# Kernel tuning notes

Measured on AMD Instinct MI355X. Metric: run time of the kernel, lower is better.

Reference implementation:

```python
import jax, jax.numpy as jnp
import numpy as np

KV_CACHE_SIZE = 8192
DIM = 128
BBPM_MEM_SIZE = 131072
B, T = 32, 8192
N_TOKENS = B * T  # 262144


def setup_inputs() -> dict:
    key = jax.random.key(0)
    k1, k2, k3 = jax.random.split(key, 3)
    keys = jax.random.randint(k1, (B, T), 0, 1000000, dtype=jnp.int64)
    values = jax.random.normal(k2, (B, T, DIM), dtype=jnp.float32)
    positions = jnp.arange(N_TOKENS, dtype=jnp.int64).reshape(B, T)
    query_keys = jax.random.randint(k3, (B, T), 0, 1000000, dtype=jnp.int64)
    query_positions = jax.random.randint(
        jax.random.fold_in(key, 7), (B, T), 0, N_TOKENS, dtype=jnp.int64)
    bbpm_mem = jnp.zeros((BBPM_MEM_SIZE, DIM), dtype=jnp.float32)
    return {"keys": keys, "values": values, "positions": positions,
            "query_keys": query_keys, "query_positions": query_positions,
            "bbpm_mem": bbpm_mem}


def reference(keys, values, positions, query_keys, query_positions, bbpm_mem):
    # --- write_to_cache ---
    keys_f = keys.reshape(-1)                  # [n]
    vals_f = values.reshape(-1, DIM)           # [n, d]
    pos_f = positions.reshape(-1)              # [n]
    n = keys_f.shape[0]

    # BBPM write: hashed additive associative memory (scatter-add).
    mem = bbpm_mem.at[keys_f % BBPM_MEM_SIZE].add(vals_f)

    # Ring-cache write: cache_ptr starts at 0 and K | n, so the sequential
    # overwrite loop leaves exactly the last K tokens: slot idx holds token
    # i = n - K + idx. (Original writes values into both k_cache and v_cache;
    # only v_cache is read.)
    K = KV_CACHE_SIZE
    v_cache = vals_f[n - K:]                   # [K, d]
    cache_positions = pos_f[n - K:]            # [K], unique

    # --- retrieve ---
    qkeys = query_keys.reshape(-1)             # [Q]
    qpos = query_positions.reshape(-1)         # [Q]

    # Position -> cache-slot map (positions are unique, so scatter-set is
    # equivalent to taking the first matching slot).
    pos_table = jnp.full((N_TOKENS,), -1, dtype=jnp.int32)
    pos_table = pos_table.at[cache_positions].set(
        jnp.arange(K, dtype=jnp.int32))
    idx = pos_table[qpos]                      # [Q]
    hit = idx >= 0

    cache_vals = v_cache[jnp.maximum(idx, 0)]          # [Q, d]
    bbpm_vals = mem[qkeys % BBPM_MEM_SIZE]             # [Q, d]
    out = jnp.where(hit[:, None], cache_vals, bbpm_vals)  # [Q, d]
    return out
```

## Files before the change

### kernel.cpp

```cpp
#include <hip/hip_runtime.h>


constexpr int DIM    = 128;
constexpr int MEM    = 131072;
constexpr int KCACHE = 8192;
constexpr int CAP    = 16;

__device__ __forceinline__ float4 ldrow(const float* __restrict__ p, int q) {
    return *reinterpret_cast<const float4*>(p + q * 4);
}

__global__ void fill_kernel(const int* __restrict__ keys,
                            int* __restrict__ cnt,
                            int* __restrict__ bucket,
                            int* __restrict__ ovf_cnt,
                            int* __restrict__ ovf,
                            int n) {
    int i = blockIdx.x * 256 + threadIdx.x;
    if (i >= n) return;
    int slot = ((unsigned)keys[i]) & (MEM - 1);
    int pos = atomicAdd(&cnt[slot], 1);
    if (pos < CAP) {
        bucket[slot * CAP + pos] = i;
    } else {
        int k = atomicAdd(ovf_cnt, 1);
        ovf[k] = i;
    }
}

__global__ void build_pos_kernel(const int* __restrict__ positions,
                                 int* __restrict__ pos_table, int n, int K) {
    int j = blockIdx.x * 256 + threadIdx.x;
    if (j >= K) return;
    int p = positions[n - K + j];
    if (p >= 0 && p < n) pos_table[p] = j;
}

__global__ void reduce_kernel(const float* __restrict__ vals,
                              const float* __restrict__ bbpm,
                              const int* __restrict__ cnt,
                              const int* __restrict__ bucket,
                              float* __restrict__ acc) {
    int g = threadIdx.x >> 5;
    int q = threadIdx.x & 31;
    int s0 = blockIdx.x * 16 + g;
    int s1 = s0 + 8;

    int c0 = cnt[s0]; if (c0 > CAP) c0 = CAP;
    int c1 = cnt[s1]; if (c1 > CAP) c1 = CAP;
    int4 b0 = reinterpret_cast<const int4*>(bucket)[s0 * 4];
    int4 b1 = reinterpret_cast<const int4*>(bucket)[s1 * 4];

    int r00 = c0 > 0 ? b0.x : 0, r01 = c0 > 1 ? b0.y : 0;
    int r10 = c1 > 0 ? b1.x : 0, r11 = c1 > 1 ? b1.y : 0;
    float m00 = c0 > 0 ? 1.f : 0.f, m01 = c0 > 1 ? 1.f : 0.f;
    float m10 = c1 > 0 ? 1.f : 0.f, m11 = c1 > 1 ? 1.f : 0.f;

    float4 A0  = ldrow(bbpm + (size_t)s0  * DIM, q);
    float4 A1  = ldrow(bbpm + (size_t)s1  * DIM, q);
    float4 V00 = ldrow(vals + (size_t)r00 * DIM, q);
    float4 V01 = ldrow(vals + (size_t)r01 * DIM, q);
    float4 V10 = ldrow(vals + (size_t)r10 * DIM, q);
    float4 V11 = ldrow(vals + (size_t)r11 * DIM, q);

    float4 a0, a1;
    a0.x = A0.x + m00 * V00.x + m01 * V01.x;
    a0.y = A0.y + m00 * V00.y + m01 * V01.y;
    a0.z = A0.z + m00 * V00.z + m01 * V01.z;
    a0.w = A0.w + m00 * V00.w + m01 * V01.w;
    a1.x = A1.x + m10 * V10.x + m11 * V11.x;
    a1.y = A1.y + m10 * V10.y + m11 * V11.y;
    a1.z = A1.z + m10 * V10.z + m11 * V11.z;
    a1.w = A1.w + m10 * V10.w + m11 * V11.w;

    if (c0 > 2) {
        float4 v = ldrow(vals + (size_t)b0.z * DIM, q);
        a0.x += v.x; a0.y += v.y; a0.z += v.z; a0.w += v.w;
        if (c0 > 3) {
            v = ldrow(vals + (size_t)b0.w * DIM, q);
            a0.x += v.x; a0.y += v.y; a0.z += v.z; a0.w += v.w;
            for (int j = 4; j < c0; ++j) {
                int r = bucket[s0 * CAP + j];
                v = ldrow(vals + (size_t)r * DIM, q);
                a0.x += v.x; a0.y += v.y; a0.z += v.z; a0.w += v.w;
            }
        }
    }
    if (c1 > 2) {
        float4 v = ldrow(vals + (size_t)b1.z * DIM, q);
        a1.x += v.x; a1.y += v.y; a1.z += v.z; a1.w += v.w;
        if (c1 > 3) {
            v = ldrow(vals + (size_t)b1.w * DIM, q);
            a1.x += v.x; a1.y += v.y; a1.z += v.z; a1.w += v.w;
            for (int j = 4; j < c1; ++j) {
                int r = bucket[s1 * CAP + j];
                v = ldrow(vals + (size_t)r * DIM, q);
                a1.x += v.x; a1.y += v.y; a1.z += v.z; a1.w += v.w;
            }
        }
    }

    *reinterpret_cast<float4*>(acc + (size_t)s0 * DIM + q * 4) = a0;
    *reinterpret_cast<float4*>(acc + (size_t)s1 * DIM + q * 4) = a1;
}

__global__ void overflow_kernel(const float* __restrict__ vals,
                                const int* __restrict__ keys,
                                const int* __restrict__ ovf_cnt,
                                const int* __restrict__ ovf,
                                float* __restrict__ acc) {
    int total = *ovf_cnt;
    int tid = blockIdx.x * 256 + threadIdx.x;
    int stride = gridDim.x * 256;
    for (int w = tid; w < total * 32; w += stride) {
        int e = w >> 5, q = w & 31;
        int i = ovf[e];
        int slot = ((unsigned)keys[i]) & (MEM - 1);
        float4 v = ldrow(vals + (size_t)i * DIM, q);
        float* dst = acc + (size_t)slot * DIM + q * 4;
        atomicAdd(dst + 0, v.x);
        atomicAdd(dst + 1, v.y);
        atomicAdd(dst + 2, v.z);
        atomicAdd(dst + 3, v.w);
    }
}

__global__ void gather_kernel(const float* __restrict__ vals,
                              const float* __restrict__ acc,
                              const int* __restrict__ qkeys,
                              const int* __restrict__ qpos,
                              const int* __restrict__ pos_table,
                              float* __restrict__ out, int n, int base) {
    int g = threadIdx.x >> 5;
    int q = threadIdx.x & 31;
    int r0 = blockIdx.x * 32 + g;
    int r1 = r0 + 8, r2 = r0 + 16, r3 = r0 + 24;

    bool k0 = r0 < n, k1 = r1 < n, k2 = r2 < n, k3 = r3 < n;
    int qp0 = k0 ? qpos[r0] : -1, qp1 = k1 ? qpos[r1] : -1;
    int qp2 = k2 ? qpos[r2] : -1, qp3 = k3 ? qpos[r3] : -1;
    int qk0 = k0 ? qkeys[r0] : 0, qk1 = k1 ? qkeys[r1] : 0;
    int qk2 = k2 ? qkeys[r2] : 0, qk3 = k3 ? qkeys[r3] : 0;

    int i0 = (qp0 >= 0 && qp0 < n) ? pos_table[qp0] : -1;
    int i1 = (qp1 >= 0 && qp1 < n) ? pos_table[qp1] : -1;
    int i2 = (qp2 >= 0 && qp2 < n) ? pos_table[qp2] : -1;
    int i3 = (qp3 >= 0 && qp3 < n) ? pos_table[qp3] : -1;

    const float* s0 = (i0 >= 0) ? vals + (size_t)(base + i0) * DIM
                                : acc + (size_t)(((unsigned)qk0) & (MEM - 1)) * DIM;
    const float* s1 = (i1 >= 0) ? vals + (size_t)(base + i1) * DIM
                                : acc + (size_t)(((unsigned)qk1) & (MEM - 1)) * DIM;
    const float* s2 = (i2 >= 0) ? vals + (size_t)(base + i2) * DIM
                                : acc + (size_t)(((unsigned)qk2) & (MEM - 1)) * DIM;
    const float* s3 = (i3 >= 0) ? vals + (size_t)(base + i3) * DIM
                                : acc + (size_t)(((unsigned)qk3) & (MEM - 1)) * DIM;

    float4 v0 = ldrow(s0, q);
    float4 v1 = ldrow(s1, q);
    float4 v2 = ldrow(s2, q);
    float4 v3 = ldrow(s3, q);

    if (k0) *reinterpret_cast<float4*>(out + (size_t)r0 * DIM + q * 4) = v0;
    if (k1) *reinterpret_cast<float4*>(out + (size_t)r1 * DIM + q * 4) = v1;
    if (k2) *reinterpret_cast<float4*>(out + (size_t)r2 * DIM + q * 4) = v2;
    if (k3) *reinterpret_cast<float4*>(out + (size_t)r3 * DIM + q * 4) = v3;
}

extern "C" void kernel_launch(void* const* d_in, const int* in_sizes, int n_in,
                              void* d_out, int out_size, void* d_ws, size_t ws_size,
                              hipStream_t stream) {
    const int*   keys      = (const int*)d_in[0];
    const float* vals      = (const float*)d_in[1];
    const int*   positions = (const int*)d_in[2];
    const int*   qkeys     = (const int*)d_in[3];
    const int*   qpos      = (const int*)d_in[4];
    const float* bbpm      = (const float*)d_in[5];
    float* out = (float*)d_out;

    const int n = in_sizes[0];
    const size_t acc_bytes = (size_t)MEM * DIM * sizeof(float);

    char* ws = (char*)d_ws;
    float* acc       = (float*)ws;
    int*   pos_table = (int*)(ws + acc_bytes);
    int*   cnt       = (int*)(ws + acc_bytes + (size_t)n * 4);
    int*   ovf_cnt   = (int*)((char*)cnt + (size_t)MEM * 4);
    int*   ovf       = (int*)((char*)ovf_cnt + 256);

    int* bucket = (int*)d_out;

    hipMemsetAsync(cnt, 0, (size_t)MEM * 4 + 256, stream);
    hipMemsetAsync(pos_table, 0xFF, (size_t)n * sizeof(int), stream);

    fill_kernel<<<(n + 255) / 256, 256, 0, stream>>>(keys, cnt, bucket, ovf_cnt, ovf, n);
    build_pos_kernel<<<(KCACHE + 255) / 256, 256, 0, stream>>>(positions, pos_table, n, KCACHE);
    reduce_kernel<<<MEM / 16, 256, 0, stream>>>(vals, bbpm, cnt, bucket, acc);
    overflow_kernel<<<64, 256, 0, stream>>>(vals, keys, ovf_cnt, ovf, acc);
    gather_kernel<<<(n + 31) / 32, 256, 0, stream>>>(vals, acc, qkeys, qpos, pos_table,
                                                     out, n, n - KCACHE);
}
```

Baseline: 135.0 us.

## Skip reduction for unqueried slots, prefetch values, use nontemporal access

A new pass marks which memory slots are actually read by queries that miss the ring cache. The reduce kernel then skips slot pairs where neither slot is marked and skips the value loads for unmarked slots. Other changes in the same edit: bucket capacity drops from 16 to 8, the bucket array moves from the output buffer into the workspace, a full pass over the values tensor is added to warm the cache, and the bbpm loads and the output stores become nontemporal. With random keys most slots are still queried, so the skip may save little. The extra flag pass and the full prefetch read add memory traffic of their own.

```diff
diff --git a/kernel.cpp b/kernel.cpp
--- a/kernel.cpp
+++ b/kernel.cpp
@@ -1,31 +1,33 @@
 #include <hip/hip_runtime.h>
 
+
+typedef float f32x4 __attribute__((ext_vector_type(4)));
+typedef int   i32x4 __attribute__((ext_vector_type(4)));
 
 constexpr int DIM    = 128;
 constexpr int MEM    = 131072;
 constexpr int KCACHE = 8192;
-constexpr int CAP    = 16;
-
-__device__ __forceinline__ float4 ldrow(const float* __restrict__ p, int q) {
-    return *reinterpret_cast<const float4*>(p + q * 4);
+constexpr int CAP    = 8;
+
+__device__ __forceinline__ f32x4 ldrow(const float* __restrict__ p, int q) {
+    return *reinterpret_cast<const f32x4*>(p + q * 4);
+}
+__device__ __forceinline__ f32x4 nt_ldrow(const float* __restrict__ p, int q) {
+    return __builtin_nontemporal_load(reinterpret_cast<const f32x4*>(p) + q);
+}
+__device__ __forceinline__ void nt_strow(float* __restrict__ p, int q, f32x4 v) {
+    __builtin_nontemporal_store(v, reinterpret_cast<f32x4*>(p) + q);
 }
 
 __global__ void fill_kernel(const int* __restrict__ keys,
-                            int* __restrict__ cnt,
-                            int* __restrict__ bucket,
-                            int* __restrict__ ovf_cnt,
-                            int* __restrict__ ovf,
-                            int n) {
+                            int* __restrict__ cnt, int* __restrict__ bucket,
+                            int* __restrict__ ovf_cnt, int* __restrict__ ovf, int n) {
     int i = blockIdx.x * 256 + threadIdx.x;
     if (i >= n) return;
     int slot = ((unsigned)keys[i]) & (MEM - 1);
     int pos = atomicAdd(&cnt[slot], 1);
-    if (pos < CAP) {
-        bucket[slot * CAP + pos] = i;
-    } else {
-        int k = atomicAdd(ovf_cnt, 1);
-        ovf[k] = i;
-    }
+    if (pos < CAP) bucket[slot * CAP + pos] = i;
+    else { int k = atomicAdd(ovf_cnt, 1); ovf[k] = i; }
 }
 
 __global__ void build_pos_kernel(const int* __restrict__ positions,
@@ -36,9 +38,32 @@
     if (p >= 0 && p < n) pos_table[p] = j;
 }
 
+__global__ void qfill_kernel(const int* __restrict__ qkeys,
+                             const int* __restrict__ qpos,
+                             const int* __restrict__ pos_table,
+                             int* __restrict__ qflag, int n) {
+    int r = blockIdx.x * 256 + threadIdx.x;
+    if (r >= n) return;
+    int qp = qpos[r];
+    int idx = (qp >= 0 && qp < n) ? pos_table[qp] : -1;
+    if (idx < 0) qflag[((unsigned)qkeys[r]) & (MEM - 1)] = 1;
+}
+
+__global__ void prefetch_kernel(const f32x4* __restrict__ v4, int n4) {
+    int tid = blockIdx.x * 256 + threadIdx.x;
+    int stride = gridDim.x * 256;
+    float s = 0.f;
+    for (int t = tid; t < n4; t += stride) {
+        f32x4 v = v4[t];
+        s += v.x + v.y + v.z + v.w;
+    }
+    asm volatile("" :: "v"(s));
+}
+
 __global__ void reduce_kernel(const float* __restrict__ vals,
                               const float* __restrict__ bbpm,
                               const int* __restrict__ cnt,
+                              const int* __restrict__ qflag,
                               const int* __restrict__ bucket,
                               float* __restrict__ acc) {
     int g = threadIdx.x >> 5;
@@ -46,62 +71,50 @@
     int s0 = blockIdx.x * 16 + g;
     int s1 = s0 + 8;
 
-    int c0 = cnt[s0]; if (c0 > CAP) c0 = CAP;
-    int c1 = cnt[s1]; if (c1 > CAP) c1 = CAP;
-    int4 b0 = reinterpret_cast<const int4*>(bucket)[s0 * 4];
-    int4 b1 = reinterpret_cast<const int4*>(bucket)[s1 * 4];
+    int f0 = qflag[s0], f1 = qflag[s1];
+    if ((f0 | f1) == 0) return;
+
+    int c0 = f0 ? cnt[s0] : 0; if (c0 > CAP) c0 = CAP;
+    int c1 = f1 ? cnt[s1] : 0; if (c1 > CAP) c1 = CAP;
+    i32x4 b0 = *reinterpret_cast<const i32x4*>(bucket + s0 * CAP);
+    i32x4 b1 = *reinterpret_cast<const i32x4*>(bucket + s1 * CAP);
 
     int r00 = c0 > 0 ? b0.x : 0, r01 = c0 > 1 ? b0.y : 0;
     int r10 = c1 > 0 ? b1.x : 0, r11 = c1 > 1 ? b1.y : 0;
     float m00 = c0 > 0 ? 1.f : 0.f, m01 = c0 > 1 ? 1.f : 0.f;
     float m10 = c1 > 0 ? 1.f : 0.f, m11 = c1 > 1 ? 1.f : 0.f;
 
-    float4 A0  = ldrow(bbpm + (size_t)s0  * DIM, q);
-    float4 A1  = ldrow(bbpm + (size_t)s1  * DIM, q);
-    float4 V00 = ldrow(vals + (size_t)r00 * DIM, q);
-    float4 V01 = ldrow(vals + (size_t)r01 * DIM, q);
-    float4 V10 = ldrow(vals + (size_t)r10 * DIM, q);
-    float4 V11 = ldrow(vals + (size_t)r11 * DIM, q);
-
-    float4 a0, a1;
-    a0.x = A0.x + m00 * V00.x + m01 * V01.x;
-    a0.y = A0.y + m00 * V00.y + m01 * V01.y;
-    a0.z = A0.z + m00 * V00.z + m01 * V01.z;
-    a0.w = A0.w + m00 * V00.w + m01 * V01.w;
-    a1.x = A1.x + m10 * V10.x + m11 * V11.x;
-    a1.y = A1.y + m10 * V10.y + m11 * V11.y;
-    a1.z = A1.z + m10 * V10.z + m11 * V11.z;
-    a1.w = A1.w + m10 * V10.w + m11 * V11.w;
+    const float* bb0 = bbpm + (f0 ? (size_t)s0 * DIM : 0);
+    const float* bb1 = bbpm + (f1 ? (size_t)s1 * DIM : 0);
+    f32x4 A0  = nt_ldrow(bb0, q);
+    f32x4 A1  = nt_ldrow(bb1, q);
+    f32x4 V00 = ldrow(vals + (size_t)r00 * DIM, q);
+    f32x4 V01 = ldrow(vals + (size_t)r01 * DIM, q);
+    f32x4 V10 = ldrow(vals + (size_t)r10 * DIM, q);
+    f32x4 V11 = ldrow(vals + (size_t)r11 * DIM, q);
+
+    f32x4 a0 = A0 + m00 * V00 + m01 * V01;
+    f32x4 a1 = A1 + m10 * V10 + m11 * V11;
 
     if (c0 > 2) {
-        float4 v = ldrow(vals + (size_t)b0.z * DIM, q);
-        a0.x += v.x; a0.y += v.y; a0.z += v.z; a0.w += v.w;
+        a0 += ldrow(vals + (size_t)b0.z * DIM, q);
         if (c0 > 3) {
-            v = ldrow(vals + (size_t)b0.w * DIM, q);
-            a0.x += v.x; a0.y += v.y; a0.z += v.z; a0.w += v.w;
-            for (int j = 4; j < c0; ++j) {
-                int r = bucket[s0 * CAP + j];
-                v = ldrow(vals + (size_t)r * DIM, q);
-                a0.x += v.x; a0.y += v.y; a0.z += v.z; a0.w += v.w;
-            }
+            a0 += ldrow(vals + (size_t)b0.w * DIM, q);
+            for (int j = 4; j < c0; ++j)
+                a0 += ldrow(vals + (size_t)bucket[s0 * CAP + j] * DIM, q);
         }
     }
     if (c1 > 2) {
-        float4 v = ldrow(vals + (size_t)b1.z * DIM, q);
-        a1.x += v.x; a1.y += v.y; a1.z += v.z; a1.w += v.w;
+        a1 += ldrow(vals + (size_t)b1.z * DIM, q);
         if (c1 > 3) {
-            v = ldrow(vals + (size_t)b1.w * DIM, q);
-            a1.x += v.x; a1.y += v.y; a1.z += v.z; a1.w += v.w;
-            for (int j = 4; j < c1; ++j) {
-                int r = bucket[s1 * CAP + j];
-                v = ldrow(vals + (size_t)r * DIM, q);
-                a1.x += v.x; a1.y += v.y; a1.z += v.z; a1.w += v.w;
-            }
+            a1 += ldrow(vals + (size_t)b1.w * DIM, q);
+            for (int j = 4; j < c1; ++j)
+                a1 += ldrow(vals + (size_t)bucket[s1 * CAP + j] * DIM, q);
         }
     }
 
-    *reinterpret_cast<float4*>(acc + (size_t)s0 * DIM + q * 4) = a0;
-    *reinterpret_cast<float4*>(acc + (size_t)s1 * DIM + q * 4) = a1;
+    if (f0) *reinterpret_cast<f32x4*>(acc + (size_t)s0 * DIM + q * 4) = a0;
+    if (f1) *reinterpret_cast<f32x4*>(acc + (size_t)s1 * DIM + q * 4) = a1;
 }
 
 __global__ void overflow_kernel(const float* __restrict__ vals,
@@ -110,13 +123,12 @@
                                 const int* __restrict__ ovf,
                                 float* __restrict__ acc) {
     int total = *ovf_cnt;
-    int tid = blockIdx.x * 256 + threadIdx.x;
-    int stride = gridDim.x * 256;
+    int tid = blockIdx.x * 256 + threadIdx.x, stride = gridDim.x * 256;
     for (int w = tid; w < total * 32; w += stride) {
         int e = w >> 5, q = w & 31;
         int i = ovf[e];
         int slot = ((unsigned)keys[i]) & (MEM - 1);
-        float4 v = ldrow(vals + (size_t)i * DIM, q);
+        f32x4 v = ldrow(vals + (size_t)i * DIM, q);
         float* dst = acc + (size_t)slot * DIM + q * 4;
         atomicAdd(dst + 0, v.x);
         atomicAdd(dst + 1, v.y);
@@ -156,15 +168,15 @@
     const float* s3 = (i3 >= 0) ? vals + (size_t)(base + i3) * DIM
                                 : acc + (size_t)(((unsigned)qk3) & (MEM - 1)) * DIM;
 
-    float4 v0 = ldrow(s0, q);
-    float4 v1 = ldrow(s1, q);
-    float4 v2 = ldrow(s2, q);
-    float4 v3 = ldrow(s3, q);
-
-    if (k0) *reinterpret_cast<float4*>(out + (size_t)r0 * DIM + q * 4) = v0;
-    if (k1) *reinterpret_cast<float4*>(out + (size_t)r1 * DIM + q * 4) = v1;
-    if (k2) *reinterpret_cast<float4*>(out + (size_t)r2 * DIM + q * 4) = v2;
-    if (k3) *reinterpret_cast<float4*>(out + (size_t)r3 * DIM + q * 4) = v3;
+    f32x4 v0 = ldrow(s0, q);
+    f32x4 v1 = ldrow(s1, q);
+    f32x4 v2 = ldrow(s2, q);
+    f32x4 v3 = ldrow(s3, q);
+
+    if (k0) nt_strow(out + (size_t)r0 * DIM, q, v0);
+    if (k1) nt_strow(out + (size_t)r1 * DIM, q, v1);
+    if (k2) nt_strow(out + (size_t)r2 * DIM, q, v2);
+    if (k3) nt_strow(out + (size_t)r3 * DIM, q, v3);
 }
 
 extern "C" void kernel_launch(void* const* d_in, const int* in_sizes, int n_in,
@@ -179,24 +191,25 @@
     float* out = (float*)d_out;
 
     const int n = in_sizes[0];
-    const size_t acc_bytes = (size_t)MEM * DIM * sizeof(float);
 
     char* ws = (char*)d_ws;
-    float* acc       = (float*)ws;
-    int*   pos_table = (int*)(ws + acc_bytes);
-    int*   cnt       = (int*)(ws + acc_bytes + (size_t)n * 4);
-    int*   ovf_cnt   = (int*)((char*)cnt + (size_t)MEM * 4);
-    int*   ovf       = (int*)((char*)ovf_cnt + 256);
-
-    int* bucket = (int*)d_out;
-
-    hipMemsetAsync(cnt, 0, (size_t)MEM * 4 + 256, stream);
-    hipMemsetAsync(pos_table, 0xFF, (size_t)n * sizeof(int), stream);
-
-    fill_kernel<<<(n + 255) / 256, 256, 0, stream>>>(keys, cnt, bucket, ovf_cnt, ovf, n);
+    int*   cnt       = (int*)ws;
+    int*   qflag     = cnt + MEM;
+    int*   ctrs      = qflag + MEM;
+    int*   pos_table = ctrs + 64;
+    int*   bucket    = pos_table + n;
+    int*   ovf       = bucket + MEM * CAP;
+    float* acc       = (float*)(ovf + n);
+
+    hipMemsetAsync(cnt, 0, (size_t)(2 * MEM + 64) * 4, stream);
+    hipMemsetAsync(pos_table, 0xFF, (size_t)n * 4, stream);
+
+    fill_kernel<<<(n + 255) / 256, 256, 0, stream>>>(keys, cnt, bucket, &ctrs[0], ovf, n);
     build_pos_kernel<<<(KCACHE + 255) / 256, 256, 0, stream>>>(positions, pos_table, n, KCACHE);
-    reduce_kernel<<<MEM / 16, 256, 0, stream>>>(vals, bbpm, cnt, bucket, acc);
-    overflow_kernel<<<64, 256, 0, stream>>>(vals, keys, ovf_cnt, ovf, acc);
+    qfill_kernel<<<(n + 255) / 256, 256, 0, stream>>>(qkeys, qpos, pos_table, qflag, n);
+    prefetch_kernel<<<2048, 256, 0, stream>>>((const f32x4*)vals, n * (DIM / 4));
+    reduce_kernel<<<MEM / 16, 256, 0, stream>>>(vals, bbpm, cnt, qflag, bucket, acc);
+    overflow_kernel<<<64, 256, 0, stream>>>(vals, keys, &ctrs[0], ovf, acc);
     gather_kernel<<<(n + 31) / 32, 256, 0, stream>>>(vals, acc, qkeys, qpos, pos_table,
                                                      out, n, n - KCACHE);
 }
```

Measured after the change: 133.4 us. Within noise of the previous version (-1.2%).
